# Kernel optimization log

Hardware: AMD Instinct MI355X
Metric: run time of the kernel (lower is better)

The kernel has to match this reference:

```python
import jax, jax.numpy as jnp
import numpy as np

N_NODES = 50000
N_EDGES = 800000
IN_CH = 64
OC = 16  # out_channels


def setup_inputs() -> dict:
    key = jax.random.key(0)
    ks = jax.random.split(key, 16)
    x = jax.random.normal(ks[0], (N_NODES, IN_CH), dtype=jnp.float32)
    edge_index = jax.random.randint(ks[1], (2, N_EDGES), 0, N_NODES, dtype=jnp.int64)

    def lin(k, fan_in, fan_out):
        s = 1.0 / np.sqrt(fan_in)
        return jax.random.uniform(k, (fan_in, fan_out), jnp.float32, -s, s)

    d1, d2 = 16 * OC, 8 * OC  # 256, 128
    return {
        "x": x,
        "W1_rel": lin(ks[2], IN_CH, d1), "b1": jnp.zeros((d1,), jnp.float32), "W1_root": lin(ks[3], IN_CH, d1),
        "W2_rel": lin(ks[4], d1, d2), "b2": jnp.zeros((d2,), jnp.float32), "W2_root": lin(ks[5], d1, d2),
        "Wmu_rel": lin(ks[6], d2, OC), "bmu": jnp.zeros((OC,), jnp.float32), "Wmu_root": lin(ks[7], d2, OC),
        "Wls_rel": lin(ks[8], d2, OC), "bls": jnp.zeros((OC,), jnp.float32), "Wls_root": lin(ks[9], d2, OC),
        "edge_index": edge_index,
    }


def _graph_conv(x, src, dst, deg_inv, W_rel, b, W_root):
    # PyG GraphConv(aggr='mean'): out = lin_rel(mean_{j in N(i)} x_j) + lin_root(x_i)
    msg_sum = jax.ops.segment_sum(x[src], dst, num_segments=x.shape[0])  # [N, d]
    agg = msg_sum * deg_inv[:, None]
    return agg @ W_rel + b + x @ W_root


def reference(x, W1_rel, b1, W1_root, W2_rel, b2, W2_root,
              Wmu_rel, bmu, Wmu_root, Wls_rel, bls, Wls_root, edge_index):
    src, dst = edge_index[0], edge_index[1]
    deg = jax.ops.segment_sum(jnp.ones_like(dst, dtype=x.dtype), dst, num_segments=x.shape[0])
    deg_inv = jnp.where(deg > 0, 1.0 / jnp.maximum(deg, 1.0), 0.0)

    h = jax.nn.relu(_graph_conv(x, src, dst, deg_inv, W1_rel, b1, W1_root))
    h = jax.nn.relu(_graph_conv(h, src, dst, deg_inv, W2_rel, b2, W2_root))
    mu = _graph_conv(h, src, dst, deg_inv, Wmu_rel, bmu, Wmu_root)
    logstd = _graph_conv(h, src, dst, deg_inv, Wls_rel, bls, Wls_root)
    return (mu, logstd)
```

## Files before the change

kernel.cpp:

```cpp
#include <hip/hip_runtime.h>
#include <hip/hip_fp8.h>

#define N_NODES 50000
#define N_EDGES 800000
#define NBUCK 196
#define PBLK 391
#define CAP 5120

typedef unsigned short ushort_t;
typedef unsigned char uchar_t;
typedef short short8 __attribute__((ext_vector_type(8)));
typedef short short4v __attribute__((ext_vector_type(4)));
typedef float floatx4 __attribute__((ext_vector_type(4)));
typedef float floatx2 __attribute__((ext_vector_type(2)));

__device__ __forceinline__ float bf2f(ushort_t u) {
    unsigned v = ((unsigned)u) << 16;
    return __builtin_bit_cast(float, v);
}
__device__ __forceinline__ ushort_t f2bf(float f) {
    unsigned u = __builtin_bit_cast(unsigned, f);
    unsigned r = (u + 0x7FFFu + ((u >> 16) & 1u)) >> 16;
    return (ushort_t)r;
}
__device__ __forceinline__ uchar_t f2fp8(float f) {
    return (uchar_t)(__builtin_amdgcn_cvt_pk_fp8_f32(f, f, 0, false) & 0xFF);
}
__device__ __forceinline__ float4 ld4(const float* p) { return *(const float4*)p; }

__device__ __forceinline__ void acc16(float* a, uint4 v) {
    unsigned ws[4] = {v.x, v.y, v.z, v.w};
    #pragma unroll
    for (int wi = 0; wi < 4; ++wi) {
        floatx2 lo = __builtin_amdgcn_cvt_pk_f32_fp8(ws[wi], false);
        floatx2 hi = __builtin_amdgcn_cvt_pk_f32_fp8(ws[wi], true);
        a[wi * 4 + 0] += lo.x; a[wi * 4 + 1] += lo.y;
        a[wi * 4 + 2] += hi.x; a[wi * 4 + 3] += hi.y;
    }
}
__device__ __forceinline__ void acc8(float* a, uint2 v) {
    floatx2 p0 = __builtin_amdgcn_cvt_pk_f32_fp8(v.x, false);
    floatx2 p1 = __builtin_amdgcn_cvt_pk_f32_fp8(v.x, true);
    floatx2 p2 = __builtin_amdgcn_cvt_pk_f32_fp8(v.y, false);
    floatx2 p3 = __builtin_amdgcn_cvt_pk_f32_fp8(v.y, true);
    a[0] += p0.x; a[1] += p0.y; a[2] += p1.x; a[3] += p1.y;
    a[4] += p2.x; a[5] += p2.y; a[6] += p3.x; a[7] += p3.y;
}

__global__ __launch_bounds__(256) void prep_kernel(
    const float* __restrict__ x,
    const float* __restrict__ W1_rel, const float* __restrict__ W1_root,
    const float* __restrict__ W2_rel, const float* __restrict__ W2_root,
    const float* __restrict__ Wmu_rel, const float* __restrict__ Wls_rel,
    const float* __restrict__ Wmu_root, const float* __restrict__ Wls_root,
    ushort_t* __restrict__ xb, uchar_t* __restrict__ xq,
    ushort_t* __restrict__ B1t, ushort_t* __restrict__ B2t, ushort_t* __restrict__ B3t,
    int* __restrict__ bcursor) {
    int idx = blockIdx.x * blockDim.x + threadIdx.x;
    if (idx < 400000) {
        int n = idx >> 3, c = (idx & 7) * 8;
        float4 v0 = ld4(x + (size_t)n * 64 + c);
        float4 v1 = ld4(x + (size_t)n * 64 + c + 4);
        float vv[8] = {v0.x, v0.y, v0.z, v0.w, v1.x, v1.y, v1.z, v1.w};
        short8 o;
        #pragma unroll
        for (int i = 0; i < 8; ++i) o[i] = f2bf(vv[i]);
        int q0 = __builtin_amdgcn_cvt_pk_fp8_f32(vv[0], vv[1], 0, false);
        q0 = __builtin_amdgcn_cvt_pk_fp8_f32(vv[2], vv[3], q0, true);
        int q1 = __builtin_amdgcn_cvt_pk_fp8_f32(vv[4], vv[5], 0, false);
        q1 = __builtin_amdgcn_cvt_pk_fp8_f32(vv[6], vv[7], q1, true);
        *(short8*)(xb + (size_t)n * 64 + c) = o;
        uint2 q = {(unsigned)q0, (unsigned)q1};
        *(uint2*)(xq + (size_t)n * 64 + c) = q;
    } else if (idx < 506496) {
        int j = idx - 400000;
        if (j < 32768) {
            int n = j >> 7, k = j & 127;
            float v = (k < 64) ? W1_rel[k * 256 + n] : W1_root[(k - 64) * 256 + n];
            B1t[j] = f2bf(v);
        } else if (j < 98304) {
            int jj = j - 32768;
            int n = jj >> 8, k = jj & 255;
            float v = (n < 128) ? W2_rel[k * 128 + n] : W2_root[k * 128 + (n - 128)];
            B2t[jj] = f2bf(v);
        } else {
            int jj = j - 98304;
            int n = jj >> 7, k = jj & 127;
            const float* W = (n < 16) ? Wmu_rel : (n < 32) ? Wls_rel : (n < 48) ? Wmu_root : Wls_root;
            B3t[jj] = f2bf(W[k * 16 + (n & 15)]);
        }
    } else if (idx < 506496 + NBUCK) {
        int b = idx - 506496;
        bcursor[b] = b * CAP;
    }
}

__global__ __launch_bounds__(512) void partition_kernel(
    const int* __restrict__ src, const int* __restrict__ dst,
    int* __restrict__ bcursor, unsigned* __restrict__ pairbuf) {
    __shared__ int h[NBUCK];
    __shared__ int cur[NBUCK];
    const int tid = threadIdx.x;
    for (int i = tid; i < NBUCK; i += 512) h[i] = 0;
    __syncthreads();
    const int base = blockIdx.x * 2048;
    int d[4];
    #pragma unroll
    for (int j = 0; j < 4; ++j) {
        int e = base + j * 512 + tid;
        if (e < N_EDGES) { d[j] = dst[e]; atomicAdd(&h[d[j] >> 8], 1); }
        else d[j] = -1;
    }
    __syncthreads();
    for (int i = tid; i < NBUCK; i += 512) {
        int c = h[i];
        cur[i] = c ? atomicAdd(&bcursor[i], c) : 0;
    }
    __syncthreads();
    #pragma unroll
    for (int j = 0; j < 4; ++j) {
        int e = base + j * 512 + tid;
        if (e < N_EDGES) {
            int dd = d[j];
            int slot = atomicAdd(&cur[dd >> 8], 1);
            pairbuf[slot] = (unsigned)src[e] | ((unsigned)(dd & 255) << 16);
        }
    }
}

__global__ __launch_bounds__(1024) void fill_bucket_kernel(
    const unsigned* __restrict__ pairbuf, const int* __restrict__ bcursor,
    int* __restrict__ row_beg, int* __restrict__ row_end,
    float* __restrict__ dinv, ushort_t* __restrict__ eidx) {
    __shared__ int h[256];
    __shared__ int sm[256];
    __shared__ int cur[256];
    const int b = blockIdx.x, tid = threadIdx.x;
    const int beg = b * CAP, end = bcursor[b];
    if (tid < 256) h[tid] = 0;
    __syncthreads();
    for (int i = beg + tid; i < end; i += 1024)
        atomicAdd(&h[pairbuf[i] >> 16], 1);
    __syncthreads();
    if (tid < 256) sm[tid] = h[tid];
    __syncthreads();
    #pragma unroll
    for (int off = 1; off < 256; off <<= 1) {
        int t = 0;
        if (tid < 256 && tid >= off) t = sm[tid - off];
        __syncthreads();
        if (tid < 256) sm[tid] += t;
        __syncthreads();
    }
    if (tid < 256) {
        int c = h[tid];
        int exc = beg + sm[tid] - c;
        int node = b * 256 + tid;
        if (node < N_NODES) {
            row_beg[node] = exc;
            row_end[node] = exc + c;
            dinv[node] = c > 0 ? 1.0f / (float)c : 0.0f;
        }
        cur[tid] = exc;
    }
    __syncthreads();
    for (int i = beg + tid; i < end; i += 1024) {
        unsigned v = pairbuf[i];
        int slot = atomicAdd(&cur[v >> 16], 1);
        eidx[slot] = (ushort_t)(v & 0xFFFFu);
    }
}

__global__ __launch_bounds__(256, 3) void g1gemm12(
    const ushort_t* __restrict__ xb, const uchar_t* __restrict__ xq,
    const int* __restrict__ row_beg, const int* __restrict__ row_end,
    const ushort_t* __restrict__ eidx, const float* __restrict__ dinv,
    const ushort_t* __restrict__ B1t, const float* __restrict__ b1,
    const ushort_t* __restrict__ B2t,
    uchar_t* __restrict__ t2, ushort_t* __restrict__ r2) {
    constexpr int K1 = 128, K2 = 256;
    constexpr int AKP = 72;
    constexpr int HKP = 264;
    constexpr int BKP = 136;
    __shared__ ushort_t Bs[64 * BKP];
    __shared__ ushort_t Hs[64 * HKP];
    ushort_t* As = Bs;
    const int tid = threadIdx.x;
    const int rowbase = blockIdx.x * 64;

    {
        const int nl = tid >> 2, lane = tid & 3;
        const int node = rowbase + nl;
        int beg = 0, end = 0;
        float d = 0.0f;
        if (node < N_NODES) { beg = row_beg[node]; end = row_end[node]; d = dinv[node]; }
        float a0[16] = {}, a1[16] = {};
        int j = beg;
        for (; j + 3 < end; j += 4) {
            uint4 v0 = *(const uint4*)(xq + (size_t)eidx[j] * 64 + lane * 16);
            uint4 v1 = *(const uint4*)(xq + (size_t)eidx[j + 1] * 64 + lane * 16);
            uint4 v2 = *(const uint4*)(xq + (size_t)eidx[j + 2] * 64 + lane * 16);
            uint4 v3 = *(const uint4*)(xq + (size_t)eidx[j + 3] * 64 + lane * 16);
            acc16(a0, v0); acc16(a1, v1); acc16(a0, v2); acc16(a1, v3);
        }
        for (; j < end; ++j) {
            uint4 v0 = *(const uint4*)(xq + (size_t)eidx[j] * 64 + lane * 16);
            acc16(a0, v0);
        }
        short8 o0, o1;
        #pragma unroll
        for (int i = 0; i < 8; ++i) {
            o0[i] = f2bf((a0[i] + a1[i]) * d);
            o1[i] = f2bf((a0[8 + i] + a1[8 + i]) * d);
        }
        *(short8*)(As + nl * AKP + lane * 16) = o0;
        *(short8*)(As + nl * AKP + lane * 16 + 8) = o1;
    }
    __syncthreads();

    const int w = tid >> 6, lane64 = tid & 63;
    const int ln = lane64 & 15, quad = lane64 >> 4;
    const int rwl = w * 16 + ln;
    int r = rowbase + rwl;
    if (r > N_NODES - 1) r = N_NODES - 1;

    float bias[4][4];
    #pragma unroll
    for (int ny = 0; ny < 4; ++ny)
        #pragma unroll
        for (int f = 0; f < 4; ++f)
            bias[ny][f] = b1[ny * 64 + f * 16 + ln];

    short8 a[4];
    a[0] = *(const short8*)(As + rwl * AKP + quad * 8);
    a[1] = *(const short8*)(As + rwl * AKP + 32 + quad * 8);
    a[2] = *(const short8*)(xb + (size_t)r * 64 + quad * 8);
    a[3] = *(const short8*)(xb + (size_t)r * 64 + 32 + quad * 8);
    {
        short8 pb[4];
        #pragma unroll
        for (int i = 0; i < 4; ++i) {
            int idx = tid + i * 256, row = idx >> 4, off = (idx & 15) * 8;
            pb[i] = *(const short8*)(B1t + (size_t)row * K1 + off);
        }
        for (int ny = 0; ny < 4; ++ny) {
            __syncthreads();
            #pragma unroll
            for (int i = 0; i < 4; ++i) {
                int idx = tid + i * 256, row = idx >> 4, off = (idx & 15) * 8;
                *(short8*)(Bs + row * BKP + off) = pb[i];
            }
            if (ny < 3) {
                #pragma unroll
                for (int i = 0; i < 4; ++i) {
                    int idx = tid + i * 256, row = idx >> 4, off = (idx & 15) * 8;
                    pb[i] = *(const short8*)(B1t + (size_t)((ny + 1) * 64 + row) * K1 + off);
                }
            }
            __syncthreads();
            floatx4 acc[4] = {};
            #pragma unroll
            for (int f = 0; f < 4; ++f) {
                const ushort_t* bp = Bs + (f * 16 + ln) * BKP + quad * 8;
                #pragma unroll
                for (int s = 0; s < 4; ++s) {
                    short8 b = *(const short8*)(bp + s * 32);
                    acc[f] = __builtin_amdgcn_mfma_f32_16x16x32_bf16(a[s], b, acc[f], 0, 0, 0);
                }
            }
            #pragma unroll
            for (int f = 0; f < 4; ++f) {
                int n = ny * 64 + f * 16 + ln;
                #pragma unroll
                for (int g = 0; g < 4; ++g) {
                    int rr = w * 16 + quad * 4 + g;
                    Hs[rr * HKP + n] = f2bf(fmaxf(acc[f][g] + bias[ny][f], 0.0f));
                }
            }
        }
    }
    __syncthreads();

    short8 a2[8];
    #pragma unroll
    for (int s = 0; s < 8; ++s)
        a2[s] = *(const short8*)(Hs + rwl * HKP + s * 32 + quad * 8);
    ushort_t* Or16 = Hs;
    uchar_t*  Ot8  = (uchar_t*)(Hs + 8704);
    {
        short8 pb[4];
        #pragma unroll
        for (int i = 0; i < 4; ++i) {
            int idx = tid + i * 256, row = idx >> 4, off = (idx & 15) * 8;
            pb[i] = *(const short8*)(B2t + (size_t)row * K2 + off);
        }
        for (int ny = 0; ny < 4; ++ny) {
            floatx4 acc[4] = {};
            #pragma unroll
            for (int kh = 0; kh < 2; ++kh) {
                __syncthreads();
                #pragma unroll
                for (int i = 0; i < 4; ++i) {
                    int idx = tid + i * 256, row = idx >> 4, off = (idx & 15) * 8;
                    *(short8*)(Bs + row * BKP + off) = pb[i];
                }
                int st = ny * 2 + kh;
                if (st < 7) {
                    int nyn = (st + 1) >> 1, khn = (st + 1) & 1;
                    #pragma unroll
                    for (int i = 0; i < 4; ++i) {
                        int idx = tid + i * 256, row = idx >> 4, off = (idx & 15) * 8;
                        pb[i] = *(const short8*)(B2t + (size_t)(nyn * 64 + row) * K2 + khn * 128 + off);
                    }
                }
                __syncthreads();
                #pragma unroll
                for (int f = 0; f < 4; ++f) {
                    const ushort_t* bp = Bs + (f * 16 + ln) * BKP + quad * 8;
                    #pragma unroll
                    for (int s = 0; s < 4; ++s) {
                        short8 b = *(const short8*)(bp + s * 32);
                        acc[f] = __builtin_amdgcn_mfma_f32_16x16x32_bf16(a2[kh * 4 + s], b, acc[f], 0, 0, 0);
                    }
                }
            }
            #pragma unroll
            for (int f = 0; f < 4; ++f) {
                int n = ny * 64 + f * 16 + ln;
                #pragma unroll
                for (int g = 0; g < 4; ++g) {
                    int rr = w * 16 + quad * 4 + g;
                    float v = acc[f][g];
                    if (n < 128) Ot8[rr * 144 + n] = f2fp8(v);
                    else Or16[rr * 136 + (n - 128)] = f2bf(v);
                }
            }
        }
    }
    __syncthreads();

    {
        const int row = tid >> 2, seg = tid & 3;
        const int gr = rowbase + row;
        if (gr < N_NODES) {
            const uint4* ps = (const uint4*)(Ot8 + row * 144 + seg * 32);
            uint4* pd = (uint4*)(t2 + (size_t)gr * 128 + seg * 32);
            pd[0] = ps[0]; pd[1] = ps[1];
            const uint4* qs = (const uint4*)(Or16 + row * 136 + seg * 32);
            uint4* qd = (uint4*)(r2 + (size_t)gr * 128 + seg * 32);
            qd[0] = qs[0]; qd[1] = qs[1]; qd[2] = qs[2]; qd[3] = qs[3];
        }
    }
}

__global__ __launch_bounds__(256) void g2g3_kernel(
    const uchar_t* __restrict__ t2, const ushort_t* __restrict__ r2,
    const int* __restrict__ row_beg, const int* __restrict__ row_end,
    const ushort_t* __restrict__ eidx, const float* __restrict__ dinv,
    const float* __restrict__ b2, const ushort_t* __restrict__ B3t,
    ushort_t* __restrict__ tml, float* __restrict__ rml) {
    constexpr int KP = 136;
    __shared__ ushort_t As[16 * KP];
    const int tid = threadIdx.x;
    const int nb = blockIdx.x * 16;
    {
        const int nl = tid >> 4, lane = tid & 15;
        const int node = nb + nl;
        const int beg = row_beg[node], end = row_end[node];
        float a0[8] = {}, a1[8] = {}, a2[8] = {}, a3[8] = {};
        int j = beg;
        for (; j + 3 < end; j += 4) {
            uint2 v0 = *(const uint2*)(t2 + (size_t)eidx[j] * 128 + lane * 8);
            uint2 v1 = *(const uint2*)(t2 + (size_t)eidx[j + 1] * 128 + lane * 8);
            uint2 v2 = *(const uint2*)(t2 + (size_t)eidx[j + 2] * 128 + lane * 8);
            uint2 v3 = *(const uint2*)(t2 + (size_t)eidx[j + 3] * 128 + lane * 8);
            acc8(a0, v0); acc8(a1, v1); acc8(a2, v2); acc8(a3, v3);
        }
        for (; j < end; ++j) {
            uint2 v0 = *(const uint2*)(t2 + (size_t)eidx[j] * 128 + lane * 8);
            acc8(a0, v0);
        }
        float d = dinv[node];
        short8 rv = *(const short8*)(r2 + (size_t)node * 128 + lane * 8);
        float4 ba = ld4(b2 + lane * 8), bb = ld4(b2 + lane * 8 + 4);
        float bc[8] = {ba.x, ba.y, ba.z, ba.w, bb.x, bb.y, bb.z, bb.w};
        short8 o;
        #pragma unroll
        for (int i = 0; i < 8; ++i)
            o[i] = f2bf(fmaxf(((a0[i] + a1[i]) + (a2[i] + a3[i])) * d + bf2f((ushort_t)rv[i]) + bc[i], 0.0f));
        *(short8*)(As + nl * KP + lane * 8) = o;
    }
    __syncthreads();
    const int w = tid >> 6, lane64 = tid & 63;
    const int ln = lane64 & 15, quad = lane64 >> 4;
    short8 a[4];
    #pragma unroll
    for (int s = 0; s < 4; ++s)
        a[s] = *(const short8*)(As + ln * KP + s * 32 + quad * 8);
    floatx4 acc = {};
    const ushort_t* bp = B3t + (size_t)(w * 16 + ln) * 128 + quad * 8;
    #pragma unroll
    for (int s = 0; s < 4; ++s) {
        short8 b = *(const short8*)(bp + s * 32);
        acc = __builtin_amdgcn_mfma_f32_16x16x32_bf16(a[s], b, acc, 0, 0, 0);
    }
    const int r0 = nb + quad * 4;
    const int ncol = w * 16 + ln;
    #pragma unroll
    for (int g = 0; g < 4; ++g) {
        int rr = r0 + g;
        float v = acc[g];
        if (ncol < 32) tml[(size_t)rr * 32 + ncol] = f2bf(v);
        else rml[(size_t)rr * 32 + (ncol - 32)] = v;
    }
}

__global__ __launch_bounds__(256) void gather3_kernel(
    const ushort_t* __restrict__ tml, const float* __restrict__ rml,
    const int* __restrict__ row_beg, const int* __restrict__ row_end,
    const ushort_t* __restrict__ eidx, const float* __restrict__ dinv,
    const float* __restrict__ bmu, const float* __restrict__ bls,
    float* __restrict__ out) {
    const int lane = threadIdx.x & 7;
    const int nl = threadIdx.x >> 3;
    const int n = blockIdx.x * 32 + nl;
    if (n >= N_NODES) return;
    const int beg = row_beg[n], end = row_end[n];
    float a0[4] = {}, a1[4] = {}, a2[4] = {}, a3[4] = {};
    int j = beg;
    for (; j + 3 < end; j += 4) {
        short4v v0 = *(const short4v*)(tml + (size_t)eidx[j] * 32 + lane * 4);
        short4v v1 = *(const short4v*)(tml + (size_t)eidx[j + 1] * 32 + lane * 4);
        short4v v2 = *(const short4v*)(tml + (size_t)eidx[j + 2] * 32 + lane * 4);
        short4v v3 = *(const short4v*)(tml + (size_t)eidx[j + 3] * 32 + lane * 4);
        #pragma unroll
        for (int i = 0; i < 4; ++i) {
            a0[i] += bf2f((ushort_t)v0[i]); a1[i] += bf2f((ushort_t)v1[i]);
            a2[i] += bf2f((ushort_t)v2[i]); a3[i] += bf2f((ushort_t)v3[i]);
        }
    }
    for (; j < end; ++j) {
        short4v v0 = *(const short4v*)(tml + (size_t)eidx[j] * 32 + lane * 4);
        #pragma unroll
        for (int i = 0; i < 4; ++i) a0[i] += bf2f((ushort_t)v0[i]);
    }
    float d = dinv[n];
    const float* bias = (lane < 4) ? (bmu + lane * 4) : (bls + (lane - 4) * 4);
    float4 ra = ld4(rml + (size_t)n * 32 + lane * 4);
    float4 ba = ld4(bias);
    float rr[4] = {ra.x, ra.y, ra.z, ra.w};
    float bc[4] = {ba.x, ba.y, ba.z, ba.w};
    float res[4];
    #pragma unroll
    for (int i = 0; i < 4; ++i) res[i] = ((a0[i] + a1[i]) + (a2[i] + a3[i])) * d + rr[i] + bc[i];
    float* base = (lane < 4) ? (out + (size_t)n * 16 + lane * 4)
                             : (out + 800000u + (size_t)n * 16 + (lane - 4) * 4);
    *(float4*)(base) = make_float4(res[0], res[1], res[2], res[3]);
}

extern "C" void kernel_launch(void* const* d_in, const int* in_sizes, int n_in,
                              void* d_out, int out_size, void* d_ws, size_t ws_size,
                              hipStream_t stream) {
    const float* x       = (const float*)d_in[0];
    const float* W1_rel  = (const float*)d_in[1];
    const float* b1      = (const float*)d_in[2];
    const float* W1_root = (const float*)d_in[3];
    const float* W2_rel  = (const float*)d_in[4];
    const float* b2      = (const float*)d_in[5];
    const float* W2_root = (const float*)d_in[6];
    const float* Wmu_rel = (const float*)d_in[7];
    const float* bmu     = (const float*)d_in[8];
    const float* Wmu_root= (const float*)d_in[9];
    const float* Wls_rel = (const float*)d_in[10];
    const float* bls     = (const float*)d_in[11];
    const float* Wls_root= (const float*)d_in[12];
    const int*   ei      = (const int*)d_in[13];
    const int* src = ei;
    const int* dst = ei + N_EDGES;

    int*      bcursor = (int*)d_ws;
    int*      row_beg = bcursor + 256;
    int*      row_end = row_beg + 50048;
    unsigned* pairbuf = (unsigned*)(row_end + 50048);
    ushort_t* eidx    = (ushort_t*)(pairbuf + 1003520);
    float*    dinv    = (float*)(eidx + 1003520);
    ushort_t* xb   = (ushort_t*)(dinv + 50000);
    uchar_t*  xq   = (uchar_t*)(xb + 3200000);
    uchar_t*  t2   = xq + 3200000;
    ushort_t* r2   = (ushort_t*)(t2 + 6400000);
    ushort_t* tml  = r2 + 6400000;
    ushort_t* B1t  = tml + 1600000;
    ushort_t* B2t  = B1t + 32768;
    ushort_t* B3t  = B2t + 65536;
    float* rml     = (float*)(B3t + 8192);
    float* out     = (float*)d_out;

    prep_kernel<<<1980, 256, 0, stream>>>(x, W1_rel, W1_root, W2_rel, W2_root,
                                          Wmu_rel, Wls_rel, Wmu_root, Wls_root,
                                          xb, xq, B1t, B2t, B3t, bcursor);
    partition_kernel<<<PBLK, 512, 0, stream>>>(src, dst, bcursor, pairbuf);
    fill_bucket_kernel<<<NBUCK, 1024, 0, stream>>>(pairbuf, bcursor, row_beg, row_end, dinv, eidx);

    g1gemm12<<<782, 256, 0, stream>>>(xb, xq, row_beg, row_end, eidx, dinv,
                                      B1t, b1, B2t, t2, r2);

    g2g3_kernel<<<3125, 256, 0, stream>>>(t2, r2, row_beg, row_end, eidx, dinv, b2, B3t, tml, rml);

    gather3_kernel<<<1563, 256, 0, stream>>>(tml, rml, row_beg, row_end, eidx, dinv, bmu, bls, out);
}
```

Baseline: 194.3 us.

## Fuse prep and edge partition kernels; unroll gather loops to eight edges

Merges the input conversion/weight transpose kernel and the edge bucketing kernel into one launch. Block ranges select the role, and the bucket cursor becomes a relative count zeroed by a memset. The partition part now uses 256-thread blocks that each handle eight edges per thread. Separately, the three neighbor gather loops gain an eight-wide unrolled stage so more independent loads are in flight. This trades launch overhead and serialization for more register pressure in the gather kernels and an extra memset call.

```diff
diff --git a/kernel.cpp b/kernel.cpp
--- a/kernel.cpp
+++ b/kernel.cpp
@@ -5,6 +5,7 @@
 #define N_EDGES 800000
 #define NBUCK 196
 #define PBLK 391
+#define PREPBLK 1980
 #define CAP 5120
 
 typedef unsigned short ushort_t;
@@ -47,79 +48,76 @@
     a[4] += p2.x; a[5] += p2.y; a[6] += p3.x; a[7] += p3.y;
 }
 
-__global__ __launch_bounds__(256) void prep_kernel(
+__global__ __launch_bounds__(256) void prep_part_kernel(
     const float* __restrict__ x,
     const float* __restrict__ W1_rel, const float* __restrict__ W1_root,
     const float* __restrict__ W2_rel, const float* __restrict__ W2_root,
     const float* __restrict__ Wmu_rel, const float* __restrict__ Wls_rel,
     const float* __restrict__ Wmu_root, const float* __restrict__ Wls_root,
+    const int* __restrict__ src, const int* __restrict__ dst,
     ushort_t* __restrict__ xb, uchar_t* __restrict__ xq,
     ushort_t* __restrict__ B1t, ushort_t* __restrict__ B2t, ushort_t* __restrict__ B3t,
-    int* __restrict__ bcursor) {
-    int idx = blockIdx.x * blockDim.x + threadIdx.x;
-    if (idx < 400000) {
-        int n = idx >> 3, c = (idx & 7) * 8;
-        float4 v0 = ld4(x + (size_t)n * 64 + c);
-        float4 v1 = ld4(x + (size_t)n * 64 + c + 4);
-        float vv[8] = {v0.x, v0.y, v0.z, v0.w, v1.x, v1.y, v1.z, v1.w};
-        short8 o;
-        #pragma unroll
-        for (int i = 0; i < 8; ++i) o[i] = f2bf(vv[i]);
-        int q0 = __builtin_amdgcn_cvt_pk_fp8_f32(vv[0], vv[1], 0, false);
-        q0 = __builtin_amdgcn_cvt_pk_fp8_f32(vv[2], vv[3], q0, true);
-        int q1 = __builtin_amdgcn_cvt_pk_fp8_f32(vv[4], vv[5], 0, false);
-        q1 = __builtin_amdgcn_cvt_pk_fp8_f32(vv[6], vv[7], q1, true);
-        *(short8*)(xb + (size_t)n * 64 + c) = o;
-        uint2 q = {(unsigned)q0, (unsigned)q1};
-        *(uint2*)(xq + (size_t)n * 64 + c) = q;
-    } else if (idx < 506496) {
-        int j = idx - 400000;
-        if (j < 32768) {
-            int n = j >> 7, k = j & 127;
-            float v = (k < 64) ? W1_rel[k * 256 + n] : W1_root[(k - 64) * 256 + n];
-            B1t[j] = f2bf(v);
-        } else if (j < 98304) {
-            int jj = j - 32768;
-            int n = jj >> 8, k = jj & 255;
-            float v = (n < 128) ? W2_rel[k * 128 + n] : W2_root[k * 128 + (n - 128)];
-            B2t[jj] = f2bf(v);
-        } else {
-            int jj = j - 98304;
-            int n = jj >> 7, k = jj & 127;
-            const float* W = (n < 16) ? Wmu_rel : (n < 32) ? Wls_rel : (n < 48) ? Wmu_root : Wls_root;
-            B3t[jj] = f2bf(W[k * 16 + (n & 15)]);
-        }
-    } else if (idx < 506496 + NBUCK) {
-        int b = idx - 506496;
-        bcursor[b] = b * CAP;
-    }
-}
-
-__global__ __launch_bounds__(512) void partition_kernel(
-    const int* __restrict__ src, const int* __restrict__ dst,
     int* __restrict__ bcursor, unsigned* __restrict__ pairbuf) {
     __shared__ int h[NBUCK];
     __shared__ int cur[NBUCK];
     const int tid = threadIdx.x;
-    for (int i = tid; i < NBUCK; i += 512) h[i] = 0;
-    __syncthreads();
-    const int base = blockIdx.x * 2048;
-    int d[4];
-    #pragma unroll
-    for (int j = 0; j < 4; ++j) {
-        int e = base + j * 512 + tid;
+    if (blockIdx.x < PREPBLK) {
+        int idx = blockIdx.x * 256 + tid;
+        if (idx < 400000) {
+            int n = idx >> 3, c = (idx & 7) * 8;
+            float4 v0 = ld4(x + (size_t)n * 64 + c);
+            float4 v1 = ld4(x + (size_t)n * 64 + c + 4);
+            float vv[8] = {v0.x, v0.y, v0.z, v0.w, v1.x, v1.y, v1.z, v1.w};
+            short8 o;
+            #pragma unroll
+            for (int i = 0; i < 8; ++i) o[i] = f2bf(vv[i]);
+            int q0 = __builtin_amdgcn_cvt_pk_fp8_f32(vv[0], vv[1], 0, false);
+            q0 = __builtin_amdgcn_cvt_pk_fp8_f32(vv[2], vv[3], q0, true);
+            int q1 = __builtin_amdgcn_cvt_pk_fp8_f32(vv[4], vv[5], 0, false);
+            q1 = __builtin_amdgcn_cvt_pk_fp8_f32(vv[6], vv[7], q1, true);
+            *(short8*)(xb + (size_t)n * 64 + c) = o;
+            uint2 q = {(unsigned)q0, (unsigned)q1};
+            *(uint2*)(xq + (size_t)n * 64 + c) = q;
+        } else if (idx < 506496) {
+            int j = idx - 400000;
+            if (j < 32768) {
+                int n = j >> 7, k = j & 127;
+                float v = (k < 64) ? W1_rel[k * 256 + n] : W1_root[(k - 64) * 256 + n];
+                B1t[j] = f2bf(v);
+            } else if (j < 98304) {
+                int jj = j - 32768;
+                int n = jj >> 8, k = jj & 255;
+                float v = (n < 128) ? W2_rel[k * 128 + n] : W2_root[k * 128 + (n - 128)];
+                B2t[jj] = f2bf(v);
+            } else {
+                int jj = j - 98304;
+                int n = jj >> 7, k = jj & 127;
+                const float* W = (n < 16) ? Wmu_rel : (n < 32) ? Wls_rel : (n < 48) ? Wmu_root : Wls_root;
+                B3t[jj] = f2bf(W[k * 16 + (n & 15)]);
+            }
+        }
+        return;
+    }
+    const int pb = blockIdx.x - PREPBLK;
+    for (int i = tid; i < NBUCK; i += 256) h[i] = 0;
+    __syncthreads();
+    const int base = pb * 2048;
+    int d[8];
+    #pragma unroll
+    for (int j = 0; j < 8; ++j) {
+        int e = base + j * 256 + tid;
         if (e < N_EDGES) { d[j] = dst[e]; atomicAdd(&h[d[j] >> 8], 1); }
         else d[j] = -1;
     }
     __syncthreads();
-    for (int i = tid; i < NBUCK; i += 512) {
+    for (int i = tid; i < NBUCK; i += 256) {
         int c = h[i];
-        cur[i] = c ? atomicAdd(&bcursor[i], c) : 0;
-    }
-    __syncthreads();
-    #pragma unroll
-    for (int j = 0; j < 4; ++j) {
-        int e = base + j * 512 + tid;
+        cur[i] = c ? (i * CAP + atomicAdd(&bcursor[i], c)) : 0;
+    }
+    __syncthreads();
+    #pragma unroll
+    for (int j = 0; j < 8; ++j) {
+        int e = base + j * 256 + tid;
         if (e < N_EDGES) {
             int dd = d[j];
             int slot = atomicAdd(&cur[dd >> 8], 1);
@@ -136,7 +134,7 @@
     __shared__ int sm[256];
     __shared__ int cur[256];
     const int b = blockIdx.x, tid = threadIdx.x;
-    const int beg = b * CAP, end = bcursor[b];
+    const int beg = b * CAP, end = beg + bcursor[b];
     if (tid < 256) h[tid] = 0;
     __syncthreads();
     for (int i = beg + tid; i < end; i += 1024)
@@ -196,6 +194,18 @@
         if (node < N_NODES) { beg = row_beg[node]; end = row_end[node]; d = dinv[node]; }
         float a0[16] = {}, a1[16] = {};
         int j = beg;
+        for (; j + 7 < end; j += 8) {
+            uint4 v0 = *(const uint4*)(xq + (size_t)eidx[j] * 64 + lane * 16);
+            uint4 v1 = *(const uint4*)(xq + (size_t)eidx[j + 1] * 64 + lane * 16);
+            uint4 v2 = *(const uint4*)(xq + (size_t)eidx[j + 2] * 64 + lane * 16);
+            uint4 v3 = *(const uint4*)(xq + (size_t)eidx[j + 3] * 64 + lane * 16);
+            uint4 v4 = *(const uint4*)(xq + (size_t)eidx[j + 4] * 64 + lane * 16);
+            uint4 v5 = *(const uint4*)(xq + (size_t)eidx[j + 5] * 64 + lane * 16);
+            uint4 v6 = *(const uint4*)(xq + (size_t)eidx[j + 6] * 64 + lane * 16);
+            uint4 v7 = *(const uint4*)(xq + (size_t)eidx[j + 7] * 64 + lane * 16);
+            acc16(a0, v0); acc16(a1, v1); acc16(a0, v2); acc16(a1, v3);
+            acc16(a0, v4); acc16(a1, v5); acc16(a0, v6); acc16(a1, v7);
+        }
         for (; j + 3 < end; j += 4) {
             uint4 v0 = *(const uint4*)(xq + (size_t)eidx[j] * 64 + lane * 16);
             uint4 v1 = *(const uint4*)(xq + (size_t)eidx[j + 1] * 64 + lane * 16);
@@ -369,6 +379,18 @@
         const int beg = row_beg[node], end = row_end[node];
         float a0[8] = {}, a1[8] = {}, a2[8] = {}, a3[8] = {};
         int j = beg;
+        for (; j + 7 < end; j += 8) {
+            uint2 v0 = *(const uint2*)(t2 + (size_t)eidx[j] * 128 + lane * 8);
+            uint2 v1 = *(const uint2*)(t2 + (size_t)eidx[j + 1] * 128 + lane * 8);
+            uint2 v2 = *(const uint2*)(t2 + (size_t)eidx[j + 2] * 128 + lane * 8);
+            uint2 v3 = *(const uint2*)(t2 + (size_t)eidx[j + 3] * 128 + lane * 8);
+            uint2 v4 = *(const uint2*)(t2 + (size_t)eidx[j + 4] * 128 + lane * 8);
+            uint2 v5 = *(const uint2*)(t2 + (size_t)eidx[j + 5] * 128 + lane * 8);
+            uint2 v6 = *(const uint2*)(t2 + (size_t)eidx[j + 6] * 128 + lane * 8);
+            uint2 v7 = *(const uint2*)(t2 + (size_t)eidx[j + 7] * 128 + lane * 8);
+            acc8(a0, v0); acc8(a1, v1); acc8(a2, v2); acc8(a3, v3);
+            acc8(a0, v4); acc8(a1, v5); acc8(a2, v6); acc8(a3, v7);
+        }
         for (; j + 3 < end; j += 4) {
             uint2 v0 = *(const uint2*)(t2 + (size_t)eidx[j] * 128 + lane * 8);
             uint2 v1 = *(const uint2*)(t2 + (size_t)eidx[j + 1] * 128 + lane * 8);
@@ -428,6 +450,23 @@
     const int beg = row_beg[n], end = row_end[n];
     float a0[4] = {}, a1[4] = {}, a2[4] = {}, a3[4] = {};
     int j = beg;
+    for (; j + 7 < end; j += 8) {
+        short4v v0 = *(const short4v*)(tml + (size_t)eidx[j] * 32 + lane * 4);
+        short4v v1 = *(const short4v*)(tml + (size_t)eidx[j + 1] * 32 + lane * 4);
+        short4v v2 = *(const short4v*)(tml + (size_t)eidx[j + 2] * 32 + lane * 4);
+        short4v v3 = *(const short4v*)(tml + (size_t)eidx[j + 3] * 32 + lane * 4);
+        short4v v4 = *(const short4v*)(tml + (size_t)eidx[j + 4] * 32 + lane * 4);
+        short4v v5 = *(const short4v*)(tml + (size_t)eidx[j + 5] * 32 + lane * 4);
+        short4v v6 = *(const short4v*)(tml + (size_t)eidx[j + 6] * 32 + lane * 4);
+        short4v v7 = *(const short4v*)(tml + (size_t)eidx[j + 7] * 32 + lane * 4);
+        #pragma unroll
+        for (int i = 0; i < 4; ++i) {
+            a0[i] += bf2f((ushort_t)v0[i]); a1[i] += bf2f((ushort_t)v1[i]);
+            a2[i] += bf2f((ushort_t)v2[i]); a3[i] += bf2f((ushort_t)v3[i]);
+            a0[i] += bf2f((ushort_t)v4[i]); a1[i] += bf2f((ushort_t)v5[i]);
+            a2[i] += bf2f((ushort_t)v6[i]); a3[i] += bf2f((ushort_t)v7[i]);
+        }
+    }
     for (; j + 3 < end; j += 4) {
         short4v v0 = *(const short4v*)(tml + (size_t)eidx[j] * 32 + lane * 4);
         short4v v1 = *(const short4v*)(tml + (size_t)eidx[j + 1] * 32 + lane * 4);
@@ -495,10 +534,10 @@
     float* rml     = (float*)(B3t + 8192);
     float* out     = (float*)d_out;
 
-    prep_kernel<<<1980, 256, 0, stream>>>(x, W1_rel, W1_root, W2_rel, W2_root,
-                                          Wmu_rel, Wls_rel, Wmu_root, Wls_root,
-                                          xb, xq, B1t, B2t, B3t, bcursor);
-    partition_kernel<<<PBLK, 512, 0, stream>>>(src, dst, bcursor, pairbuf);
+    hipMemsetAsync(bcursor, 0, 256 * sizeof(int), stream);
+    prep_part_kernel<<<PREPBLK + PBLK, 256, 0, stream>>>(
+        x, W1_rel, W1_root, W2_rel, W2_root, Wmu_rel, Wls_rel, Wmu_root, Wls_root,
+        src, dst, xb, xq, B1t, B2t, B3t, bcursor, pairbuf);
     fill_bucket_kernel<<<NBUCK, 1024, 0, stream>>>(pairbuf, bcursor, row_beg, row_end, dinv, eidx);
 
     g1gemm12<<<782, 256, 0, stream>>>(xb, xq, row_beg, row_end, eidx, dinv,
```

Measured after the change: 199.6 us. 1.03x slower.
